# Kernel tuning notes

Measured on AMD Instinct MI355X. Metric: run time of the kernel, lower is better.

The kernel has to match this reference:

```python
import jax, jax.numpy as jnp
import numpy as np

B, E, D, H = 4096, 16, 512, 2048

def setup_inputs() -> dict:
    key = jax.random.key(0)
    k1, k2, k3, k4 = jax.random.split(key, 4)
    semantic_vec = jax.random.normal(k1, (B, D), dtype=jnp.float32)
    field_centers = jax.random.normal(k2, (E, D), dtype=jnp.float32)
    # Kaiming-uniform-ish Linear init scale
    lim = 1.0 / np.sqrt(D)
    W = jax.random.uniform(k3, (E, H, D), dtype=jnp.float32, minval=-lim, maxval=lim)
    b = jax.random.uniform(k4, (E, H), dtype=jnp.float32, minval=-lim, maxval=lim)
    return {"semantic_vec": semantic_vec, "field_centers": field_centers, "W": W, "b": b}

def reference(semantic_vec, field_centers, W, b):
    # Each expert e: relu((x - c_e) @ W_e^T + b_e); sum over experts.
    # Use linearity: (x - c_e) @ W_e^T = x @ W_e^T - c_e @ W_e^T, avoiding the [B,E,D] offsets tensor.
    xw = jnp.einsum('bd,ehd->beh', semantic_vec, W)          # [B,E,H]
    cw = jnp.einsum('ed,ehd->eh', field_centers, W)          # [E,H]
    pre = xw - cw[None, :, :] + b[None, :, :]                # [B,E,H]
    feature_anchor = jnp.sum(jax.nn.relu(pre), axis=1)       # [B,H]
    return feature_anchor
```

## Files before the change

### kernel.cpp

```cpp
#include <hip/hip_runtime.h>
#include <hip/hip_bf16.h>
#include <stdint.h>
#include <stddef.h>


#define B_DIM 4096
#define E_DIM 16
#define D_DIM 512
#define H_DIM 2048

typedef short bf16x8 __attribute__((ext_vector_type(8)));
typedef float f32x4 __attribute__((ext_vector_type(4)));

__device__ __forceinline__ short f2bf(float f) {
  __hip_bfloat16 h = __float2bfloat16(f);
  return *reinterpret_cast<short*>(&h);
}

__device__ __forceinline__ bf16x8 cvt8(float4 a, float4 b) {
  bf16x8 v;
  v[0] = f2bf(a.x); v[1] = f2bf(a.y); v[2] = f2bf(a.z); v[3] = f2bf(a.w);
  v[4] = f2bf(b.x); v[5] = f2bf(b.y); v[6] = f2bf(b.z); v[7] = f2bf(b.w);
  return v;
}

__device__ __forceinline__ void async_copy16(const void* gptr, void* lptr) {
  __builtin_amdgcn_global_load_lds(
      (const __attribute__((address_space(1))) void*)gptr,
      (__attribute__((address_space(3))) void*)lptr,
      16, 0, 0);
}

__global__ __launch_bounds__(256) void prep_w(
    const float* __restrict__ W, const float* __restrict__ C,
    const float* __restrict__ bias, __hip_bfloat16* __restrict__ Wb,
    float* __restrict__ bias2) {
  const int gw = (blockIdx.x * 256 + threadIdx.x) >> 6;
  const int lane = threadIdx.x & 63;
  const int e = gw >> 11;

  const float* wr = W + (size_t)gw * D_DIM + lane * 8;
  const float* cr = C + (size_t)e * D_DIM + lane * 8;
  float4 w0 = *(const float4*)(wr);
  float4 w1 = *(const float4*)(wr + 4);
  float4 c0 = *(const float4*)(cr);
  float4 c1 = *(const float4*)(cr + 4);

  *(bf16x8*)((__hip_bfloat16*)Wb + (size_t)gw * D_DIM + lane * 8) = cvt8(w0, w1);

  float dot = w0.x * c0.x + w0.y * c0.y + w0.z * c0.z + w0.w * c0.w +
              w1.x * c1.x + w1.y * c1.y + w1.z * c1.z + w1.w * c1.w;
#pragma unroll
  for (int off = 32; off > 0; off >>= 1) dot += __shfl_down(dot, off, 64);
  if (lane == 0) bias2[gw] = bias[gw] - dot;
}

__global__ __launch_bounds__(256) void conv_x(
    const float* __restrict__ X, __hip_bfloat16* __restrict__ Xb) {
  const size_t i = ((size_t)blockIdx.x * 256 + threadIdx.x) * 8;
  float4 a = *(const float4*)(X + i);
  float4 b = *(const float4*)(X + i + 4);
  *(bf16x8*)(Xb + i) = cvt8(a, b);
}

__global__ __launch_bounds__(256, 2) void moe_gemm(
    const __hip_bfloat16* __restrict__ Xb,
    const __hip_bfloat16* __restrict__ Wb,
    const float* __restrict__ bias2,
    float* __restrict__ out) {
  __shared__ __align__(16) __hip_bfloat16 As[128 * 32];
  __shared__ __align__(16) __hip_bfloat16 Bs[128 * 32];
  __shared__ __align__(16) float biasS[E_DIM * 128];

  const int tid = threadIdx.x;
  const int lane = tid & 63;
  const int wave = tid >> 6;
  const int hi = blockIdx.x & 15;
  const int mi = blockIdx.x >> 4;
  const int m0 = mi * 128;
  const int h0 = hi * 128;

  for (int idx = tid; idx < E_DIM * 128; idx += 256) {
    biasS[idx] = bias2[((idx >> 7) << 11) + h0 + (idx & 127)];
  }

  const int wm = (wave & 1) * 64;
  const int wn = (wave >> 1) * 64;
  const int lm = lane & 15;
  const int lk = (lane >> 4) * 8;

  const int ar0 = tid >> 2;
  const int ar1 = (tid + 256) >> 2;
  const int ac = (tid & 3) << 3;

  const __hip_bfloat16* Arow0 = Xb + (size_t)(m0 + ar0) * D_DIM + ac;
  const __hip_bfloat16* Arow1 = Xb + (size_t)(m0 + ar1) * D_DIM + ac;

  f32x4 sum[4][4];
#pragma unroll
  for (int i = 0; i < 4; ++i)
#pragma unroll
    for (int j = 0; j < 4; ++j) sum[i][j] = (f32x4){0.f, 0.f, 0.f, 0.f};

  for (int e = 0; e < E_DIM; ++e) {
    const __hip_bfloat16* Wrow0 = Wb + ((size_t)e * H_DIM + h0 + ar0) * D_DIM + ac;
    const __hip_bfloat16* Wrow1 = Wb + ((size_t)e * H_DIM + h0 + ar1) * D_DIM + ac;

    f32x4 acc[4][4];
#pragma unroll
    for (int i = 0; i < 4; ++i)
#pragma unroll
      for (int j = 0; j < 4; ++j) acc[i][j] = (f32x4){0.f, 0.f, 0.f, 0.f};

    for (int k = 0; k < D_DIM; k += 32) {
      __syncthreads();
      async_copy16(Arow0 + k, &As[(size_t)tid * 8]);
      async_copy16(Arow1 + k, &As[(size_t)(tid + 256) * 8]);
      async_copy16(Wrow0 + k, &Bs[(size_t)tid * 8]);
      async_copy16(Wrow1 + k, &Bs[(size_t)(tid + 256) * 8]);
      __syncthreads();

      bf16x8 af[4], bfr[4];
#pragma unroll
      for (int i = 0; i < 4; ++i)
        af[i] = *(const bf16x8*)&As[(wm + i * 16 + lm) * 32 + lk];
#pragma unroll
      for (int j = 0; j < 4; ++j)
        bfr[j] = *(const bf16x8*)&Bs[(wn + j * 16 + lm) * 32 + lk];
#pragma unroll
      for (int i = 0; i < 4; ++i)
#pragma unroll
        for (int j = 0; j < 4; ++j)
          acc[i][j] = __builtin_amdgcn_mfma_f32_16x16x32_bf16(
              af[i], bfr[j], acc[i][j], 0, 0, 0);
    }

    float bv[4];
#pragma unroll
    for (int j = 0; j < 4; ++j) bv[j] = biasS[e * 128 + wn + j * 16 + lm];
#pragma unroll
    for (int i = 0; i < 4; ++i)
#pragma unroll
      for (int j = 0; j < 4; ++j)
#pragma unroll
        for (int r = 0; r < 4; ++r)
          sum[i][j][r] += fmaxf(acc[i][j][r] + bv[j], 0.f);
  }

  const int rbase = (lane >> 4) * 4;
#pragma unroll
  for (int i = 0; i < 4; ++i)
#pragma unroll
    for (int j = 0; j < 4; ++j)
#pragma unroll
      for (int r = 0; r < 4; ++r)
        out[(size_t)(m0 + wm + i * 16 + rbase + r) * H_DIM + h0 + wn + j * 16 + lm] =
            sum[i][j][r];
}

__global__ __launch_bounds__(256) void naive_kernel(
    const float* __restrict__ x, const float* __restrict__ c,
    const float* __restrict__ W, const float* __restrict__ bias,
    float* __restrict__ out) {
  const int idx = blockIdx.x * 256 + threadIdx.x;
  const int b = idx >> 11;
  const int h = idx & (H_DIM - 1);
  const float* xr = x + (size_t)b * D_DIM;
  float s = 0.f;
  for (int e = 0; e < E_DIM; ++e) {
    const float* wr = W + ((size_t)e * H_DIM + h) * D_DIM;
    const float* cr = c + (size_t)e * D_DIM;
    float acc = bias[e * H_DIM + h];
    for (int d = 0; d < D_DIM; ++d) acc += (xr[d] - cr[d]) * wr[d];
    s += fmaxf(acc, 0.f);
  }
  out[idx] = s;
}

extern "C" void kernel_launch(void* const* d_in, const int* in_sizes, int n_in,
                              void* d_out, int out_size, void* d_ws, size_t ws_size,
                              hipStream_t stream) {
  const float* x = (const float*)d_in[0];
  const float* c = (const float*)d_in[1];
  const float* W = (const float*)d_in[2];
  const float* b = (const float*)d_in[3];
  float* out = (float*)d_out;

  const size_t sz_wb = (size_t)E_DIM * H_DIM * D_DIM * 2;
  const size_t sz_xb = (size_t)B_DIM * D_DIM * 2;
  const size_t sz_b2 = (size_t)E_DIM * H_DIM * 4;
  const size_t need = sz_wb + sz_xb + sz_b2;

  if (ws_size >= need) {
    __hip_bfloat16* Wb = (__hip_bfloat16*)((char*)d_ws);
    __hip_bfloat16* Xb = (__hip_bfloat16*)((char*)d_ws + sz_wb);
    float* bias2 = (float*)((char*)d_ws + sz_wb + sz_xb);
    prep_w<<<8192, 256, 0, stream>>>(W, c, b, Wb, bias2);
    conv_x<<<1024, 256, 0, stream>>>(x, Xb);
    moe_gemm<<<512, 256, 0, stream>>>(Xb, Wb, bias2, out);
  } else {
    naive_kernel<<<(B_DIM * H_DIM) / 256, 256, 0, stream>>>(x, c, W, b, out);
  }
}
```

Measured before the change: 281.4 us.

## Process two experts per pass sharing A tile and swizzle LDS layout

```diff
diff --git a/kernel.cpp b/kernel.cpp
--- a/kernel.cpp
+++ b/kernel.cpp
@@ -69,7 +69,8 @@
     const float* __restrict__ bias2,
     float* __restrict__ out) {
   __shared__ __align__(16) __hip_bfloat16 As[128 * 32];
-  __shared__ __align__(16) __hip_bfloat16 Bs[128 * 32];
+  __shared__ __align__(16) __hip_bfloat16 Bs0[128 * 32];
+  __shared__ __align__(16) __hip_bfloat16 Bs1[128 * 32];
   __shared__ __align__(16) float biasS[E_DIM * 128];
 
   const int tid = threadIdx.x;
@@ -87,14 +88,31 @@
   const int wm = (wave & 1) * 64;
   const int wn = (wave >> 1) * 64;
   const int lm = lane & 15;
-  const int lk = (lane >> 4) * 8;
-
-  const int ar0 = tid >> 2;
-  const int ar1 = (tid + 256) >> 2;
-  const int ac = (tid & 3) << 3;
-
-  const __hip_bfloat16* Arow0 = Xb + (size_t)(m0 + ar0) * D_DIM + ac;
-  const __hip_bfloat16* Arow1 = Xb + (size_t)(m0 + ar1) * D_DIM + ac;
+  const int q = lane >> 4;
+
+  const int r = tid >> 2;
+  const int ql = tid & 3;
+  const int fr = (r ^ (r >> 2)) & 3;
+  const int srcCol = ((ql ^ fr) << 3);
+
+  const __hip_bfloat16* Asrc0 = Xb + (size_t)(m0 + r) * D_DIM + srcCol;
+  const __hip_bfloat16* Asrc1 = Xb + (size_t)(m0 + r + 64) * D_DIM + srcCol;
+  const size_t brow0 = (size_t)(h0 + r) * D_DIM + srcCol;
+  const size_t brow1 = (size_t)(h0 + r + 64) * D_DIM + srcCol;
+
+  int offA[4], offB[4];
+#pragma unroll
+  for (int i = 0; i < 4; ++i) {
+    const int R = wm + i * 16 + lm;
+    const int f = (R ^ (R >> 2)) & 3;
+    offA[i] = R * 32 + ((q ^ f) << 3);
+  }
+#pragma unroll
+  for (int j = 0; j < 4; ++j) {
+    const int R = wn + j * 16 + lm;
+    const int f = (R ^ (R >> 2)) & 3;
+    offB[j] = R * 32 + ((q ^ f) << 3);
+  }
 
   f32x4 sum[4][4];
 #pragma unroll
@@ -102,60 +120,69 @@
 #pragma unroll
     for (int j = 0; j < 4; ++j) sum[i][j] = (f32x4){0.f, 0.f, 0.f, 0.f};
 
-  for (int e = 0; e < E_DIM; ++e) {
-    const __hip_bfloat16* Wrow0 = Wb + ((size_t)e * H_DIM + h0 + ar0) * D_DIM + ac;
-    const __hip_bfloat16* Wrow1 = Wb + ((size_t)e * H_DIM + h0 + ar1) * D_DIM + ac;
-
-    f32x4 acc[4][4];
+  for (int ep = 0; ep < E_DIM / 2; ++ep) {
+    const __hip_bfloat16* B0 = Wb + ((size_t)(2 * ep) << 20);
+    const __hip_bfloat16* B1 = Wb + ((size_t)(2 * ep + 1) << 20);
+
+    f32x4 acc0[4][4], acc1[4][4];
 #pragma unroll
     for (int i = 0; i < 4; ++i)
 #pragma unroll
-      for (int j = 0; j < 4; ++j) acc[i][j] = (f32x4){0.f, 0.f, 0.f, 0.f};
+      for (int j = 0; j < 4; ++j) {
+        acc0[i][j] = (f32x4){0.f, 0.f, 0.f, 0.f};
+        acc1[i][j] = (f32x4){0.f, 0.f, 0.f, 0.f};
+      }
 
     for (int k = 0; k < D_DIM; k += 32) {
       __syncthreads();
-      async_copy16(Arow0 + k, &As[(size_t)tid * 8]);
-      async_copy16(Arow1 + k, &As[(size_t)(tid + 256) * 8]);
-      async_copy16(Wrow0 + k, &Bs[(size_t)tid * 8]);
-      async_copy16(Wrow1 + k, &Bs[(size_t)(tid + 256) * 8]);
+      async_copy16(Asrc0 + k, &As[(size_t)tid * 8]);
+      async_copy16(Asrc1 + k, &As[(size_t)(tid + 256) * 8]);
+      async_copy16(B0 + brow0 + k, &Bs0[(size_t)tid * 8]);
+      async_copy16(B0 + brow1 + k, &Bs0[(size_t)(tid + 256) * 8]);
+      async_copy16(B1 + brow0 + k, &Bs1[(size_t)tid * 8]);
+      async_copy16(B1 + brow1 + k, &Bs1[(size_t)(tid + 256) * 8]);
       __syncthreads();
 
-      bf16x8 af[4], bfr[4];
+      bf16x8 af[4];
+#pragma unroll
+      for (int i = 0; i < 4; ++i) af[i] = *(const bf16x8*)&As[offA[i]];
+#pragma unroll
+      for (int j = 0; j < 4; ++j) {
+        const bf16x8 b0 = *(const bf16x8*)&Bs0[offB[j]];
+#pragma unroll
+        for (int i = 0; i < 4; ++i)
+          acc0[i][j] = __builtin_amdgcn_mfma_f32_16x16x32_bf16(
+              af[i], b0, acc0[i][j], 0, 0, 0);
+        const bf16x8 b1 = *(const bf16x8*)&Bs1[offB[j]];
+#pragma unroll
+        for (int i = 0; i < 4; ++i)
+          acc1[i][j] = __builtin_amdgcn_mfma_f32_16x16x32_bf16(
+              af[i], b1, acc1[i][j], 0, 0, 0);
+      }
+    }
+
+#pragma unroll
+    for (int j = 0; j < 4; ++j) {
+      const float bv0 = biasS[(2 * ep) * 128 + wn + j * 16 + lm];
+      const float bv1 = biasS[(2 * ep + 1) * 128 + wn + j * 16 + lm];
 #pragma unroll
       for (int i = 0; i < 4; ++i)
-        af[i] = *(const bf16x8*)&As[(wm + i * 16 + lm) * 32 + lk];
-#pragma unroll
-      for (int j = 0; j < 4; ++j)
-        bfr[j] = *(const bf16x8*)&Bs[(wn + j * 16 + lm) * 32 + lk];
-#pragma unroll
-      for (int i = 0; i < 4; ++i)
-#pragma unroll
-        for (int j = 0; j < 4; ++j)
-          acc[i][j] = __builtin_amdgcn_mfma_f32_16x16x32_bf16(
-              af[i], bfr[j], acc[i][j], 0, 0, 0);
+#pragma unroll
+        for (int t = 0; t < 4; ++t)
+          sum[i][j][t] += fmaxf(acc0[i][j][t] + bv0, 0.f) +
+                          fmaxf(acc1[i][j][t] + bv1, 0.f);
     }
-
-    float bv[4];
-#pragma unroll
-    for (int j = 0; j < 4; ++j) bv[j] = biasS[e * 128 + wn + j * 16 + lm];
-#pragma unroll
-    for (int i = 0; i < 4; ++i)
-#pragma unroll
-      for (int j = 0; j < 4; ++j)
-#pragma unroll
-        for (int r = 0; r < 4; ++r)
-          sum[i][j][r] += fmaxf(acc[i][j][r] + bv[j], 0.f);
-  }
-
-  const int rbase = (lane >> 4) * 4;
+  }
+
+  const int rbase = q * 4;
 #pragma unroll
   for (int i = 0; i < 4; ++i)
 #pragma unroll
     for (int j = 0; j < 4; ++j)
 #pragma unroll
-      for (int r = 0; r < 4; ++r)
-        out[(size_t)(m0 + wm + i * 16 + rbase + r) * H_DIM + h0 + wn + j * 16 + lm] =
-            sum[i][j][r];
+      for (int t = 0; t < 4; ++t)
+        out[(size_t)(m0 + wm + i * 16 + rbase + t) * H_DIM + h0 + wn + j * 16 + lm] =
+            sum[i][j][t];
 }
 
 __global__ __launch_bounds__(256) void naive_kernel(
```

Measured after the change: 262.0 us. -6.9%, faster.
